# Kernel optimization log

Hardware: AMD Instinct MI355X
Metric: run time of the kernel (lower is better)

The kernel has to match this reference:

```python
import jax, jax.numpy as jnp
import numpy as np

DIM = 1024
H = 16
DH = 64
INNER = H * DH
SCALE = DH ** -0.5


def setup_inputs() -> dict:
    key = jax.random.key(0)
    ks = jax.random.split(key, 6)
    B, L, R = 4, 4096, 512
    x = jax.random.normal(ks[0], (B, L, DIM), dtype=jnp.float32)
    context = jax.random.normal(ks[1], (B, R, DIM), dtype=jnp.float32)
    s = DIM ** -0.5
    Wq = jax.random.normal(ks[2], (DIM, INNER), dtype=jnp.float32) * s
    Wk = jax.random.normal(ks[3], (DIM, INNER), dtype=jnp.float32) * s
    Wv = jax.random.normal(ks[4], (DIM, INNER), dtype=jnp.float32) * s
    Wo = jax.random.normal(ks[5], (INNER, DIM), dtype=jnp.float32) * (INNER ** -0.5)
    return {"x": x, "context": context, "Wq": Wq, "Wk": Wk, "Wv": Wv, "Wo": Wo}


def reference(x, context, Wq, Wk, Wv, Wo):
    B, L, _ = x.shape
    R = context.shape[1]
    # project and split heads: (B, H, L/R, Dh)
    q = (x @ Wq).reshape(B, L, H, DH).transpose(0, 2, 1, 3)
    k = (context @ Wk).reshape(B, R, H, DH).transpose(0, 2, 1, 3)
    v = (context @ Wv).reshape(B, R, H, DH).transpose(0, 2, 1, 3)
    scores = jnp.einsum('bhld,bhrd->bhlr', q, k) * SCALE  # (B,H,L,R)
    attn = jax.nn.softmax(scores, axis=-1)
    out = jnp.einsum('bhlr,bhrd->bhld', attn, v)
    out = out.transpose(0, 2, 1, 3).reshape(B, L, INNER)
    return out @ Wo
```

## Files before the change

kernel.cpp:

```cpp
#include <hip/hip_runtime.h>
#include <hip/hip_bf16.h>

#define DIMC 1024
#define HEADS 16
#define DHEAD 64
#define LQ 4096
#define RK 512
#define BATCH 4

using bf16x8  = __attribute__((ext_vector_type(8))) __bf16;
using short4v = __attribute__((ext_vector_type(4))) short;
using f32x4   = __attribute__((ext_vector_type(4))) float;

__device__ inline ushort f2bf(float f) {
  __hip_bfloat16 h = __float2bfloat16(f);
  return *reinterpret_cast<ushort*>(&h);
}

__global__ __launch_bounds__(256) void cvt_in(const float* __restrict__ x,
    const float* __restrict__ ctx, ushort* __restrict__ xb,
    ushort* __restrict__ ctxb) {
  size_t i = ((size_t)blockIdx.x * 256 + threadIdx.x) * 8;
  const float* src; ushort* dst; size_t off;
  if (i < (size_t)16777216) { src = x; dst = xb; off = i; }
  else { src = ctx; dst = ctxb; off = i - 16777216; }
  float4 a = *(const float4*)(src + off);
  float4 b = *(const float4*)(src + off + 4);
  ushort u[8];
  u[0]=f2bf(a.x); u[1]=f2bf(a.y); u[2]=f2bf(a.z); u[3]=f2bf(a.w);
  u[4]=f2bf(b.x); u[5]=f2bf(b.y); u[6]=f2bf(b.z); u[7]=f2bf(b.w);
  *(uint4*)(dst + off) = *(const uint4*)u;
}

__global__ __launch_bounds__(256) void transpose_w(const float* __restrict__ W0,
    const float* __restrict__ W1, const float* __restrict__ W2,
    const float* __restrict__ W3, ushort* __restrict__ D0,
    ushort* __restrict__ D1, ushort* __restrict__ D2, ushort* __restrict__ D3) {
  __shared__ ushort tile[32][33];
  const float* src = (blockIdx.z == 0) ? W0 : (blockIdx.z == 1) ? W1
                   : (blockIdx.z == 2) ? W2 : W3;
  ushort* dst = (blockIdx.z == 0) ? D0 : (blockIdx.z == 1) ? D1
              : (blockIdx.z == 2) ? D2 : D3;
  const int tx = threadIdx.x, ty = threadIdx.y;
  const int x = blockIdx.x * 32 + tx;
  #pragma unroll
  for (int j = 0; j < 32; j += 8)
    tile[ty + j][tx] = f2bf(src[(size_t)(blockIdx.y * 32 + ty + j) * DIMC + x]);
  __syncthreads();
  const int xo = blockIdx.y * 32 + tx;
  #pragma unroll
  for (int j = 0; j < 32; j += 8)
    dst[(size_t)(blockIdx.x * 32 + ty + j) * DIMC + xo] = tile[tx][ty + j];
}

__global__ __launch_bounds__(256) void gemm_bt(const ushort* __restrict__ A,
    const ushort* __restrict__ Bt, void* __restrict__ Cv,
    ushort* __restrict__ CV, int mode) {
  __shared__ ushort As[128 * 32];
  __shared__ ushort Bs[128 * 32];
  const int tid  = threadIdx.x;
  const int wave = tid >> 6, lane = tid & 63;
  const int lr = lane & 15, quad = lane >> 4;
  const size_t m0 = (size_t)blockIdx.y * 128;
  const size_t n0 = (size_t)blockIdx.x * 128;
  const int wm = (wave >> 1) * 64, wn = (wave & 1) * 64;
  f32x4 acc[4][4] = {};
  for (int k0 = 0; k0 < DIMC; k0 += 32) {
    __syncthreads();
    #pragma unroll
    for (int t = 0; t < 2; ++t) {
      int c = (wave * 2 + t) * 64 + lane;
      int row = c >> 2, cc = c & 3;
      const ushort* ga = A  + (m0 + row) * DIMC + k0 + cc * 8;
      const ushort* gb = Bt + (n0 + row) * DIMC + k0 + cc * 8;
      __builtin_amdgcn_global_load_lds(
          (__attribute__((address_space(1))) void*)ga,
          (__attribute__((address_space(3))) void*)(As + (size_t)(wave * 2 + t) * 512),
          16, 0, 0);
      __builtin_amdgcn_global_load_lds(
          (__attribute__((address_space(1))) void*)gb,
          (__attribute__((address_space(3))) void*)(Bs + (size_t)(wave * 2 + t) * 512),
          16, 0, 0);
    }
    __syncthreads();
    bf16x8 af[4], bfr[4];
    #pragma unroll
    for (int mt = 0; mt < 4; ++mt)
      af[mt] = *(const bf16x8*)(As + (wm + mt * 16 + lr) * 32 + quad * 8);
    #pragma unroll
    for (int nt = 0; nt < 4; ++nt)
      bfr[nt] = *(const bf16x8*)(Bs + (wn + nt * 16 + lr) * 32 + quad * 8);
    #pragma unroll
    for (int mt = 0; mt < 4; ++mt)
      #pragma unroll
      for (int nt = 0; nt < 4; ++nt)
        acc[mt][nt] = __builtin_amdgcn_mfma_f32_16x16x32_bf16(
            af[mt], bfr[nt], acc[mt][nt], 0, 0, 0);
  }
  if (mode == 1) {
    float* C32 = (float*)Cv;
    #pragma unroll
    for (int mt = 0; mt < 4; ++mt)
      #pragma unroll
      for (int nt = 0; nt < 4; ++nt)
        #pragma unroll
        for (int j = 0; j < 4; ++j) {
          size_t m = m0 + wm + mt * 16 + quad * 4 + j;
          size_t n = n0 + wn + nt * 16 + lr;
          C32[m * DIMC + n] = acc[mt][nt][j];
        }
  } else if (mode == 0 || n0 < 1024) {
    ushort* C16 = (ushort*)Cv;
    #pragma unroll
    for (int mt = 0; mt < 4; ++mt)
      #pragma unroll
      for (int nt = 0; nt < 4; ++nt)
        #pragma unroll
        for (int j = 0; j < 4; ++j) {
          size_t m = m0 + wm + mt * 16 + quad * 4 + j;
          size_t n = n0 + wn + nt * 16 + lr;
          C16[m * DIMC + n] = f2bf(acc[mt][nt][j]);
        }
  } else {
    #pragma unroll
    for (int mt = 0; mt < 4; ++mt)
      #pragma unroll
      for (int nt = 0; nt < 4; ++nt) {
        size_t m = m0 + wm + mt * 16 + quad * 4;
        int hcol = (int)(n0 + wn + nt * 16 + lr) - 1024;
        int h = hcol >> 6, dh = hcol & 63;
        int bb = (int)(m >> 9), r = (int)(m & 511);
        ushort o4[4];
        #pragma unroll
        for (int j = 0; j < 4; ++j) o4[j] = f2bf(acc[mt][nt][j]);
        *(ushort4*)(CV + (((size_t)bb * HEADS + h) * 64 + dh) * RK + r) =
            *(const ushort4*)o4;
      }
  }
}

__global__ __launch_bounds__(256) void attn(ushort* __restrict__ QO,
    const ushort* __restrict__ K, const ushort* __restrict__ Vt) {
  __shared__ __align__(16) ushort Ks[128 * 72];
  __shared__ __align__(16) ushort Vs[64 * 136];
  const int tid  = threadIdx.x;
  const int wave = tid >> 6, lane = tid & 63;
  const int lr = lane & 15, quad = lane >> 4;
  const int b = blockIdx.z, h = blockIdx.y, qb = blockIdx.x;

  bf16x8 bq[2];
  {
    size_t row = (size_t)b * LQ + qb * 64 + wave * 16 + lr;
    const ushort* qp = QO + row * DIMC + h * DHEAD + quad * 8;
    bq[0] = *(const bf16x8*)(qp);
    bq[1] = *(const bf16x8*)(qp + 32);
  }
  float mi = -1e30f, li = 0.f;
  f32x4 o[4] = {};

  for (int rc = 0; rc < 4; ++rc) {
    __syncthreads();
    #pragma unroll
    for (int i = 0; i < 4; ++i) {
      int c = i * 256 + tid;
      {
        int kr = c >> 3, kc = c & 7;
        *(uint4*)(Ks + kr * 72 + kc * 8) = *(const uint4*)(
            K + ((size_t)b * RK + rc * 128 + kr) * DIMC + h * DHEAD + kc * 8);
      }
      {
        int vr = c >> 4, vc = c & 15;
        *(uint4*)(Vs + vr * 136 + vc * 8) = *(const uint4*)(
            Vt + (((size_t)b * HEADS + h) * 64 + vr) * RK + rc * 128 + vc * 8);
      }
    }
    __syncthreads();

    float s[8][4];
    #pragma unroll
    for (int nt = 0; nt < 8; ++nt) {
      f32x4 acc = {};
      const ushort* kp = Ks + (nt * 16 + lr) * 72 + quad * 8;
      acc = __builtin_amdgcn_mfma_f32_16x16x32_bf16(*(const bf16x8*)kp,        bq[0], acc, 0, 0, 0);
      acc = __builtin_amdgcn_mfma_f32_16x16x32_bf16(*(const bf16x8*)(kp + 32), bq[1], acc, 0, 0, 0);
      #pragma unroll
      for (int j = 0; j < 4; ++j) s[nt][j] = acc[j] * 0.125f;
    }

    float cm = s[0][0];
    #pragma unroll
    for (int nt = 0; nt < 8; ++nt)
      #pragma unroll
      for (int j = 0; j < 4; ++j) cm = fmaxf(cm, s[nt][j]);
    cm = fmaxf(cm, __shfl_xor(cm, 16));
    cm = fmaxf(cm, __shfl_xor(cm, 32));
    float mnew = fmaxf(mi, cm);
    float alpha = __expf(mi - mnew);
    mi = mnew;
    float rs = 0.f;
    #pragma unroll
    for (int nt = 0; nt < 8; ++nt)
      #pragma unroll
      for (int j = 0; j < 4; ++j) {
        float p = __expf(s[nt][j] - mnew);
        s[nt][j] = p;
        rs += p;
      }
    rs += __shfl_xor(rs, 16);
    rs += __shfl_xor(rs, 32);
    li = li * alpha + rs;

    float a_bc[4];
    #pragma unroll
    for (int j = 0; j < 4; ++j) a_bc[j] = __shfl(alpha, quad * 4 + j, 16);
    #pragma unroll
    for (int n2 = 0; n2 < 4; ++n2)
      #pragma unroll
      for (int j = 0; j < 4; ++j) o[n2][j] *= a_bc[j];

    short4v pf[8];
    #pragma unroll
    for (int nt = 0; nt < 8; ++nt)
      #pragma unroll
      for (int j = 0; j < 4; ++j) pf[nt][j] = (short)f2bf(s[nt][j]);

    #pragma unroll
    for (int kt = 0; kt < 8; ++kt)
      #pragma unroll
      for (int n2 = 0; n2 < 4; ++n2) {
        short4v bv = *(const short4v*)(Vs + (n2 * 16 + lr) * 136 + kt * 16 + quad * 4);
        o[n2] = __builtin_amdgcn_mfma_f32_16x16x16bf16_1k(pf[kt], bv, o[n2], 0, 0, 0);
      }
  }

  float li_bc[4];
  #pragma unroll
  for (int j = 0; j < 4; ++j) li_bc[j] = __shfl(li, quad * 4 + j, 16);
  #pragma unroll
  for (int n2 = 0; n2 < 4; ++n2)
    #pragma unroll
    for (int j = 0; j < 4; ++j) {
      size_t row = (size_t)b * LQ + qb * 64 + wave * 16 + quad * 4 + j;
      QO[row * DIMC + h * DHEAD + n2 * 16 + lr] = f2bf(o[n2][j] / li_bc[j]);
    }
}

extern "C" void kernel_launch(void* const* d_in, const int* in_sizes, int n_in,
                              void* d_out, int out_size, void* d_ws, size_t ws_size,
                              hipStream_t stream) {
  const float* x   = (const float*)d_in[0];
  const float* ctx = (const float*)d_in[1];

  ushort* outs = (ushort*)d_out;
  ushort* xb   = outs;
  ushort* ctxb = outs + (size_t)16777216;
  ushort* WqT  = outs + (size_t)18874368;
  ushort* WkT  = outs + (size_t)19922944;
  ushort* WvT  = outs + (size_t)20971520;
  ushort* Kw   = outs + (size_t)22020096;
  ushort* Vt_g = outs + (size_t)24117248;

  ushort* ws  = (ushort*)d_ws;
  ushort* Qw  = ws;
  ushort* WoT = ws + (size_t)16384 * 1024;

  cvt_in<<<9216, 256, 0, stream>>>(x, ctx, xb, ctxb);
  transpose_w<<<dim3(32, 32, 4), dim3(32, 8), 0, stream>>>(
      (const float*)d_in[2], (const float*)d_in[3], (const float*)d_in[4],
      (const float*)d_in[5], WqT, WkT, WvT, WoT);
  gemm_bt<<<dim3(8, 128), 256, 0, stream>>>(xb,   WqT, Qw, nullptr, 0);
  gemm_bt<<<dim3(16, 16), 256, 0, stream>>>(ctxb, WkT, Kw, Vt_g,    2);
  attn<<<dim3(LQ / 64, HEADS, BATCH), 256, 0, stream>>>(Qw, Kw, Vt_g);
  gemm_bt<<<dim3(8, 128), 256, 0, stream>>>(Qw, WoT, d_out, nullptr, 1);
}
```

Baseline: 371.6 us.

## Prefetch K/V into registers, fold softmax scale into Q, lazy rescale, swizzle GEMM grid

The attention kernel now prefetches the next K/V chunk into registers while computing the current one. It folds SCALE·log2(e) into the Q projection epilogue so it can use raw exp2 (v_exp_f32), and skips the output rescale when the running max grows by at most 8. It also pads the V LDS stride and raises wave priority around the MFMA blocks. The GEMM remaps block indices in groups of 8 to improve L2 locality. Together these reduce load latency and ALU work in softmax, at the cost of more registers and a bounded overflow margin in the lazy-rescale path.

```diff
diff --git a/kernel.cpp b/kernel.cpp
--- a/kernel.cpp
+++ b/kernel.cpp
@@ -8,6 +8,8 @@
 #define RK 512
 #define BATCH 4
 
+#define QSCALE 0.18033688011112042f
+
 using bf16x8  = __attribute__((ext_vector_type(8))) __bf16;
 using short4v = __attribute__((ext_vector_type(4))) short;
 using f32x4   = __attribute__((ext_vector_type(4))) float;
@@ -15,6 +17,10 @@
 __device__ inline ushort f2bf(float f) {
   __hip_bfloat16 h = __float2bfloat16(f);
   return *reinterpret_cast<ushort*>(&h);
+}
+
+__device__ inline float exp2_fast(float x) {
+  float r; asm("v_exp_f32 %0, %1" : "=v"(r) : "v"(x)); return r;
 }
 
 __global__ __launch_bounds__(256) void cvt_in(const float* __restrict__ x,
@@ -61,8 +67,13 @@
   const int tid  = threadIdx.x;
   const int wave = tid >> 6, lane = tid & 63;
   const int lr = lane & 15, quad = lane >> 4;
-  const size_t m0 = (size_t)blockIdx.y * 128;
-  const size_t n0 = (size_t)blockIdx.x * 128;
+  const int nbx = gridDim.x;
+  const int bid = blockIdx.y * nbx + blockIdx.x;
+  const int cpx = (nbx * gridDim.y) >> 3;
+  const int swz = (bid & 7) * cpx + (bid >> 3);
+  const int bx = swz % nbx, by = swz / nbx;
+  const size_t m0 = (size_t)by * 128;
+  const size_t n0 = (size_t)bx * 128;
   const int wm = (wave >> 1) * 64, wn = (wave & 1) * 64;
   f32x4 acc[4][4] = {};
   for (int k0 = 0; k0 < DIMC; k0 += 32) {
@@ -110,6 +121,7 @@
           C32[m * DIMC + n] = acc[mt][nt][j];
         }
   } else if (mode == 0 || n0 < 1024) {
+    const float scl = (mode == 0) ? QSCALE : 1.0f;
     ushort* C16 = (ushort*)Cv;
     #pragma unroll
     for (int mt = 0; mt < 4; ++mt)
@@ -119,7 +131,7 @@
         for (int j = 0; j < 4; ++j) {
           size_t m = m0 + wm + mt * 16 + quad * 4 + j;
           size_t n = n0 + wn + nt * 16 + lr;
-          C16[m * DIMC + n] = f2bf(acc[mt][nt][j]);
+          C16[m * DIMC + n] = f2bf(acc[mt][nt][j] * scl);
         }
   } else {
     #pragma unroll
@@ -142,7 +154,7 @@
 __global__ __launch_bounds__(256) void attn(ushort* __restrict__ QO,
     const ushort* __restrict__ K, const ushort* __restrict__ Vt) {
   __shared__ __align__(16) ushort Ks[128 * 72];
-  __shared__ __align__(16) ushort Vs[64 * 136];
+  __shared__ __align__(16) ushort Vs[64 * 140];
   const int tid  = threadIdx.x;
   const int wave = tid >> 6, lane = tid & 63;
   const int lr = lane & 15, quad = lane >> 4;
@@ -155,6 +167,22 @@
     bq[0] = *(const bf16x8*)(qp);
     bq[1] = *(const bf16x8*)(qp + 32);
   }
+
+  const int krow = tid >> 3, kcol = (tid & 7) * 8;
+  const int vrow = tid >> 4, vcol = (tid & 15) * 8;
+  const ushort* Kbase = K  + ((size_t)b * RK) * DIMC + h * DHEAD;
+  const ushort* Vbase = Vt + (((size_t)b * HEADS + h) * 64) * RK;
+
+  uint4 kreg[4], vreg[4];
+  auto issue = [&](int rc) {
+    #pragma unroll
+    for (int i = 0; i < 4; ++i) {
+      kreg[i] = *(const uint4*)(Kbase + (size_t)(rc * 128 + i * 32 + krow) * DIMC + kcol);
+      vreg[i] = *(const uint4*)(Vbase + (size_t)(i * 16 + vrow) * RK + rc * 128 + vcol);
+    }
+  };
+  issue(0);
+
   float mi = -1e30f, li = 0.f;
   f32x4 o[4] = {};
 
@@ -162,21 +190,14 @@
     __syncthreads();
     #pragma unroll
     for (int i = 0; i < 4; ++i) {
-      int c = i * 256 + tid;
-      {
-        int kr = c >> 3, kc = c & 7;
-        *(uint4*)(Ks + kr * 72 + kc * 8) = *(const uint4*)(
-            K + ((size_t)b * RK + rc * 128 + kr) * DIMC + h * DHEAD + kc * 8);
-      }
-      {
-        int vr = c >> 4, vc = c & 15;
-        *(uint4*)(Vs + vr * 136 + vc * 8) = *(const uint4*)(
-            Vt + (((size_t)b * HEADS + h) * 64 + vr) * RK + rc * 128 + vc * 8);
-      }
+      *(uint4*)(Ks + (i * 32 + krow) * 72 + kcol)  = kreg[i];
+      *(uint4*)(Vs + (i * 16 + vrow) * 140 + vcol) = vreg[i];
     }
     __syncthreads();
+    if (rc < 3) issue(rc + 1);
 
     float s[8][4];
+    __builtin_amdgcn_s_setprio(1);
     #pragma unroll
     for (int nt = 0; nt < 8; ++nt) {
       f32x4 acc = {};
@@ -184,53 +205,60 @@
       acc = __builtin_amdgcn_mfma_f32_16x16x32_bf16(*(const bf16x8*)kp,        bq[0], acc, 0, 0, 0);
       acc = __builtin_amdgcn_mfma_f32_16x16x32_bf16(*(const bf16x8*)(kp + 32), bq[1], acc, 0, 0, 0);
       #pragma unroll
-      for (int j = 0; j < 4; ++j) s[nt][j] = acc[j] * 0.125f;
-    }
-
-    float cm = s[0][0];
-    #pragma unroll
-    for (int nt = 0; nt < 8; ++nt)
-      #pragma unroll
-      for (int j = 0; j < 4; ++j) cm = fmaxf(cm, s[nt][j]);
+      for (int j = 0; j < 4; ++j) s[nt][j] = acc[j];
+    }
+    __builtin_amdgcn_s_setprio(0);
+
+    float c0 = s[0][0], c1 = s[0][1], c2 = s[0][2], c3 = s[0][3];
+    #pragma unroll
+    for (int nt = 1; nt < 8; ++nt) {
+      c0 = fmaxf(c0, s[nt][0]); c1 = fmaxf(c1, s[nt][1]);
+      c2 = fmaxf(c2, s[nt][2]); c3 = fmaxf(c3, s[nt][3]);
+    }
+    float cm = fmaxf(fmaxf(c0, c1), fmaxf(c2, c3));
     cm = fmaxf(cm, __shfl_xor(cm, 16));
     cm = fmaxf(cm, __shfl_xor(cm, 32));
-    float mnew = fmaxf(mi, cm);
-    float alpha = __expf(mi - mnew);
-    mi = mnew;
-    float rs = 0.f;
-    #pragma unroll
-    for (int nt = 0; nt < 8; ++nt)
-      #pragma unroll
-      for (int j = 0; j < 4; ++j) {
-        float p = __expf(s[nt][j] - mnew);
-        s[nt][j] = p;
-        rs += p;
-      }
+
+    if (!__all(cm - mi <= 8.f)) {
+      float mnew = fmaxf(mi, cm);
+      float alpha = exp2_fast(mi - mnew);
+      mi = mnew;
+      li *= alpha;
+      float a_bc[4];
+      #pragma unroll
+      for (int j = 0; j < 4; ++j) a_bc[j] = __shfl(alpha, quad * 4 + j, 16);
+      #pragma unroll
+      for (int n2 = 0; n2 < 4; ++n2)
+        #pragma unroll
+        for (int j = 0; j < 4; ++j) o[n2][j] *= a_bc[j];
+    }
+
+    short4v pf[8];
+    float r0 = 0.f, r1 = 0.f, r2 = 0.f, r3 = 0.f;
+    #pragma unroll
+    for (int nt = 0; nt < 8; ++nt) {
+      float p0 = exp2_fast(s[nt][0] - mi);
+      float p1 = exp2_fast(s[nt][1] - mi);
+      float p2 = exp2_fast(s[nt][2] - mi);
+      float p3 = exp2_fast(s[nt][3] - mi);
+      r0 += p0; r1 += p1; r2 += p2; r3 += p3;
+      pf[nt][0] = (short)f2bf(p0); pf[nt][1] = (short)f2bf(p1);
+      pf[nt][2] = (short)f2bf(p2); pf[nt][3] = (short)f2bf(p3);
+    }
+    float rs = (r0 + r1) + (r2 + r3);
     rs += __shfl_xor(rs, 16);
     rs += __shfl_xor(rs, 32);
-    li = li * alpha + rs;
-
-    float a_bc[4];
-    #pragma unroll
-    for (int j = 0; j < 4; ++j) a_bc[j] = __shfl(alpha, quad * 4 + j, 16);
-    #pragma unroll
-    for (int n2 = 0; n2 < 4; ++n2)
-      #pragma unroll
-      for (int j = 0; j < 4; ++j) o[n2][j] *= a_bc[j];
-
-    short4v pf[8];
-    #pragma unroll
-    for (int nt = 0; nt < 8; ++nt)
-      #pragma unroll
-      for (int j = 0; j < 4; ++j) pf[nt][j] = (short)f2bf(s[nt][j]);
-
+    li += rs;
+
+    __builtin_amdgcn_s_setprio(1);
     #pragma unroll
     for (int kt = 0; kt < 8; ++kt)
       #pragma unroll
       for (int n2 = 0; n2 < 4; ++n2) {
-        short4v bv = *(const short4v*)(Vs + (n2 * 16 + lr) * 136 + kt * 16 + quad * 4);
+        short4v bv = *(const short4v*)(Vs + (n2 * 16 + lr) * 140 + kt * 16 + quad * 4);
         o[n2] = __builtin_amdgcn_mfma_f32_16x16x16bf16_1k(pf[kt], bv, o[n2], 0, 0, 0);
       }
+    __builtin_amdgcn_s_setprio(0);
   }
 
   float li_bc[4];
```

Result: slower. 424.5 us (+14.2%).
